# Kernel optimization log

Hardware: AMD Instinct MI355X
Metric: run time of the kernel (lower is better)

The kernel has to match this reference:

```python
import jax, jax.numpy as jnp
import numpy as np
from jax import lax

BS, SL, T = 1024, 512, 64


def setup_inputs() -> dict:
    key = jax.random.key(0)
    k_e, k_tags, k_st, k_et, k_t = jax.random.split(key, 5)
    e = jax.random.normal(k_e, (BS, SL, T), dtype=jnp.float32)
    tags = jax.random.randint(k_tags, (BS, SL), 0, T, dtype=jnp.int32)
    mask = jnp.ones((BS, SL), dtype=bool)
    st = jax.random.uniform(k_st, (T,), minval=-0.1, maxval=0.1, dtype=jnp.float32)
    et = jax.random.uniform(k_et, (T,), minval=-0.1, maxval=0.1, dtype=jnp.float32)
    t = jax.random.uniform(k_t, (T, T), minval=-0.1, maxval=0.1, dtype=jnp.float32)
    return {"e": e, "tags": tags, "mask": mask, "st": st, "et": et, "t": t}


def reference(e, tags, mask, st, et, t):
    # time-major: [sl, bs, T], [sl, bs], [sl, bs]
    e_t = jnp.transpose(e, (1, 0, 2))
    tags_t = tags.T
    mask_t = mask.T
    sl, bs = tags_t.shape
    idx = jnp.arange(bs)

    # gold path score and partition-function init at step 0
    score0 = st[tags_t[0]] + e_t[0, idx, tags_t[0]]          # [bs]
    norm0 = st[None, :] + e_t[0]                              # [bs, T]

    def step(carry, xs):
        score, normalize = carry
        tag_prev, tag_next, e_next, m_next = xs
        mf = m_next.astype(e_next.dtype)
        score = score + (t[tag_prev, tag_next] + e_next[idx, tag_next]) * mf
        # logsumexp over previous tag: [bs, T_prev, T_next] -> [bs, T_next]
        ns = jax.nn.logsumexp(normalize[:, :, None] + t[None, :, :] + e_next[:, None, :], axis=1)
        normalize = jnp.where(m_next[:, None], ns, normalize)
        return (score, normalize), None

    xs = (tags_t[:-1], tags_t[1:], e_t[1:], mask_t[1:])
    (score, normalize), _ = lax.scan(step, (score0, norm0), xs)

    last = mask_t.sum(axis=0) - 1                             # [bs]
    score = score + et[tags_t[last, idx]]
    logZ = jax.nn.logsumexp(normalize + et[None, :], axis=1)  # [bs]
    total = mask.sum().astype(e.dtype)
    return (score - logZ).sum() / total
```

## Files before the change

### kernel.cpp

```cpp
#include <hip/hip_runtime.h>

#define BS 1024
#define SL 512
#define T  64

typedef float v2f __attribute__((ext_vector_type(2)));

__device__ __forceinline__ float wave_reduce_max(float x) {
#pragma unroll
    for (int m = 32; m >= 1; m >>= 1) x = fmaxf(x, __shfl_xor(x, m, 64));
    return x;
}
__device__ __forceinline__ float wave_reduce_sum(float x) {
#pragma unroll
    for (int m = 32; m >= 1; m >>= 1) x += __shfl_xor(x, m, 64);
    return x;
}

#define STEP(S_, EV_)                                                           \
    {                                                                           \
        const int s_ = (S_);                                                    \
        if ((s_ & 63) == 0) tgc = tb[s_ + j];                                   \
        const int tag = __builtin_amdgcn_readlane(tgc, s_ & 63);                \
        const float tv = t[(tag_prev << 6) + tag];                              \
        v2f a0 = {0.f, 0.f}, a1 = {0.f, 0.f}, a2 = {0.f, 0.f}, a3 = {0.f, 0.f}; \
        const int vb_ = __float_as_int(v);                                      \
        _Pragma("unroll")                                                       \
        for (int i = 0; i < T; i += 8) {                                        \
            v2f p0, p1, p2, p3;                                                 \
            p0.x = __int_as_float(__builtin_amdgcn_readlane(vb_, i + 0));       \
            p0.y = __int_as_float(__builtin_amdgcn_readlane(vb_, i + 1));       \
            p1.x = __int_as_float(__builtin_amdgcn_readlane(vb_, i + 2));       \
            p1.y = __int_as_float(__builtin_amdgcn_readlane(vb_, i + 3));       \
            p2.x = __int_as_float(__builtin_amdgcn_readlane(vb_, i + 4));       \
            p2.y = __int_as_float(__builtin_amdgcn_readlane(vb_, i + 5));       \
            p3.x = __int_as_float(__builtin_amdgcn_readlane(vb_, i + 6));       \
            p3.y = __int_as_float(__builtin_amdgcn_readlane(vb_, i + 7));       \
            a0 = __builtin_elementwise_fma(p0, tf2[(i >> 1) + 0], a0);          \
            a1 = __builtin_elementwise_fma(p1, tf2[(i >> 1) + 1], a1);          \
            a2 = __builtin_elementwise_fma(p2, tf2[(i >> 1) + 2], a2);          \
            a3 = __builtin_elementwise_fma(p3, tf2[(i >> 1) + 3], a3);          \
        }                                                                       \
        const float ev_ = (EV_);                                                \
        const float acc_ = ((a0.x + a0.y) + (a1.x + a1.y)) +                    \
                           ((a2.x + a2.y) + (a3.x + a3.y));                     \
        v = acc_ * __expf(ev_);                                                 \
        sc += (j == tag) ? (ev_ + tv) : 0.0f;                                   \
        tag_prev = tag;                                                         \
    }

__global__ __launch_bounds__(64, 1) __attribute__((amdgpu_waves_per_eu(1, 1)))
void crf_fused_kernel(const float* __restrict__ e, const int* __restrict__ tags,
                      const float* __restrict__ st, const float* __restrict__ et,
                      const float* __restrict__ t, float* __restrict__ ws) {
    const int b = blockIdx.x;
    const int j = threadIdx.x;
    const float* eb = e + (size_t)b * (SL * T) + j;
    const int* tb = tags + b * SL;

    v2f tf2[T / 2];
#pragma unroll
    for (int k = 0; k < T / 2; ++k) {
        v2f p;
        p.x = __expf(t[(2 * k) * T + j]);
        p.y = __expf(t[(2 * k + 1) * T + j]);
        tf2[k] = p;
    }

    int tgc = tb[j];
    int tag_prev = __builtin_amdgcn_readlane(tgc, 0);

    const float ev0 = eb[0];
    const float x0 = st[j] + ev0;
    const float m0 = wave_reduce_max(x0);
    float v = __expf(x0 - m0);
    float logscale = m0;
    float sc = (j == 0) ? st[tag_prev] : 0.0f;
    sc += (j == tag_prev) ? ev0 : 0.0f;

    float r0 = eb[1 * T], r1 = eb[2 * T], r2 = eb[3 * T], r3 = eb[4 * T];
    float r4 = eb[5 * T], r5 = eb[6 * T], r6 = eb[7 * T], r7 = eb[8 * T];
    float r8 = eb[9 * T], r9 = eb[10 * T], r10 = eb[11 * T], r11 = eb[12 * T];

    for (int base = 1; base <= SL - 4; base += 4) {
        const int q0 = min(base + 12, SL - 1), q1 = min(base + 13, SL - 1);
        const int q2 = min(base + 14, SL - 1), q3 = min(base + 15, SL - 1);
        const float n0 = eb[(size_t)q0 * T], n1 = eb[(size_t)q1 * T];
        const float n2 = eb[(size_t)q2 * T], n3 = eb[(size_t)q3 * T];

        STEP(base + 0, r0)
        STEP(base + 1, r1)
        STEP(base + 2, r2)
        STEP(base + 3, r3)

        r0 = r4;  r1 = r5;  r2 = r6;  r3 = r7;
        r4 = r8;  r5 = r9;  r6 = r10; r7 = r11;
        r8 = n0;  r9 = n1;  r10 = n2; r11 = n3;

        const int mb = __builtin_amdgcn_readfirstlane(__float_as_int(v));
        const int ex = ((mb >> 23) & 0xff) - 126;
        v *= __int_as_float((127 - ex) << 23);
        logscale += (float)ex * 0.6931471805599453f;
    }
    STEP(509, r0)
    STEP(510, r1)
    STEP(511, r2)

    sc += (j == 0) ? et[tag_prev] : 0.0f;

    const float z = v * __expf(et[j]);
    const float Z = wave_reduce_sum(z);
    const float scs = wave_reduce_sum(sc);
    if (j == 0) ws[b] = scs - (__logf(Z) + logscale);
}

__global__ __launch_bounds__(256)
void final_kernel(const float* __restrict__ ws, float* __restrict__ out) {
    const int tid = threadIdx.x;
    float x = (ws[tid] + ws[tid + 256]) + (ws[tid + 512] + ws[tid + 768]);
    x = wave_reduce_sum(x);
    __shared__ float sm[4];
    if ((tid & 63) == 0) sm[tid >> 6] = x;
    __syncthreads();
    if (tid == 0) out[0] = ((sm[0] + sm[1]) + (sm[2] + sm[3])) / (float)(BS * SL);
}

extern "C" void kernel_launch(void* const* d_in, const int* in_sizes, int n_in,
                              void* d_out, int out_size, void* d_ws, size_t ws_size,
                              hipStream_t stream) {
    const float* e    = (const float*)d_in[0];
    const int*   tags = (const int*)d_in[1];
    const float* st   = (const float*)d_in[3];
    const float* et   = (const float*)d_in[4];
    const float* t    = (const float*)d_in[5];
    float* out = (float*)d_out;
    float* ws  = (float*)d_ws;

    crf_fused_kernel<<<BS, 64, 0, stream>>>(e, tags, st, et, t, ws);
    final_kernel<<<1, 256, 0, stream>>>(ws, out);
}
```

Baseline: 301.7 us.

## Compute CRF forward recurrence matvec with bf16 MFMA instead of readlane FMAs

Replaces the per-step 64x64 scalar matvec, built from readlane broadcasts and packed FMAs, with bf16 16x16x32 MFMA instructions. exp(transitions) is kept in eight bf16 B fragments, and the state vector is re-packed into A fragments each step via ds_bpermute. This is meant to shorten the serial per-step latency of the scan. In exchange it adds an LDS-permute round trip per step and lowers the precision of both the transition matrix and the state to bf16, which can shift the result.

```diff
diff --git a/kernel.cpp b/kernel.cpp
--- a/kernel.cpp
+++ b/kernel.cpp
@@ -1,10 +1,15 @@
 #include <hip/hip_runtime.h>
+#include <hip/hip_bf16.h>
 
 #define BS 1024
 #define SL 512
 #define T  64
 
-typedef float v2f __attribute__((ext_vector_type(2)));
+typedef float f32x4 __attribute__((ext_vector_type(4)));
+typedef short bf16x8 __attribute__((ext_vector_type(8)));
+typedef int   i32x4  __attribute__((ext_vector_type(4)));
+
+union FragU { i32x4 i; bf16x8 v; };
 
 __device__ __forceinline__ float wave_reduce_max(float x) {
 #pragma unroll
@@ -17,36 +22,66 @@
     return x;
 }
 
-#define STEP(S_, EV_)                                                           \
-    {                                                                           \
-        const int s_ = (S_);                                                    \
-        if ((s_ & 63) == 0) tgc = tb[s_ + j];                                   \
-        const int tag = __builtin_amdgcn_readlane(tgc, s_ & 63);                \
-        const float tv = t[(tag_prev << 6) + tag];                              \
-        v2f a0 = {0.f, 0.f}, a1 = {0.f, 0.f}, a2 = {0.f, 0.f}, a3 = {0.f, 0.f}; \
-        const int vb_ = __float_as_int(v);                                      \
-        _Pragma("unroll")                                                       \
-        for (int i = 0; i < T; i += 8) {                                        \
-            v2f p0, p1, p2, p3;                                                 \
-            p0.x = __int_as_float(__builtin_amdgcn_readlane(vb_, i + 0));       \
-            p0.y = __int_as_float(__builtin_amdgcn_readlane(vb_, i + 1));       \
-            p1.x = __int_as_float(__builtin_amdgcn_readlane(vb_, i + 2));       \
-            p1.y = __int_as_float(__builtin_amdgcn_readlane(vb_, i + 3));       \
-            p2.x = __int_as_float(__builtin_amdgcn_readlane(vb_, i + 4));       \
-            p2.y = __int_as_float(__builtin_amdgcn_readlane(vb_, i + 5));       \
-            p3.x = __int_as_float(__builtin_amdgcn_readlane(vb_, i + 6));       \
-            p3.y = __int_as_float(__builtin_amdgcn_readlane(vb_, i + 7));       \
-            a0 = __builtin_elementwise_fma(p0, tf2[(i >> 1) + 0], a0);          \
-            a1 = __builtin_elementwise_fma(p1, tf2[(i >> 1) + 1], a1);          \
-            a2 = __builtin_elementwise_fma(p2, tf2[(i >> 1) + 2], a2);          \
-            a3 = __builtin_elementwise_fma(p3, tf2[(i >> 1) + 3], a3);          \
-        }                                                                       \
-        const float ev_ = (EV_);                                                \
-        const float acc_ = ((a0.x + a0.y) + (a1.x + a1.y)) +                    \
-                           ((a2.x + a2.y) + (a3.x + a3.y));                     \
-        v = acc_ * __expf(ev_);                                                 \
-        sc += (j == tag) ? (ev_ + tv) : 0.0f;                                   \
-        tag_prev = tag;                                                         \
+__device__ __forceinline__ int pk2(float a, float b) {
+    union { __hip_bfloat162 h; int i; } u;
+    u.h = __float22bfloat162_rn(make_float2(a, b));
+    return u.i;
+}
+
+#define MFMA16(A_, B_, C_) __builtin_amdgcn_mfma_f32_16x16x32_bf16((A_), (B_), (C_), 0, 0, 0)
+
+#define STEP(S_, EV_)                                                         \
+    {                                                                         \
+        const int s_ = (S_);                                                  \
+        if ((s_ & 63) == 0) tgc = tb[s_ + j];                                 \
+        const int tag = __builtin_amdgcn_readlane(tgc, s_ & 63);              \
+        const float tv_ = t[(tag_prev << 6) + tag];                           \
+        const float ev_ = (EV_);                                              \
+        const float ge_ = __expf(ev_);                \
+        f32x4 c0 = {0.f, 0.f, 0.f, 0.f}, c1 = {0.f, 0.f, 0.f, 0.f};          \
+        f32x4 c2 = {0.f, 0.f, 0.f, 0.f}, c3 = {0.f, 0.f, 0.f, 0.f};          \
+        c0 = MFMA16(A0, B00, c0); c1 = MFMA16(A0, B01, c1);                   \
+        c2 = MFMA16(A0, B02, c2); c3 = MFMA16(A0, B03, c3);                   \
+        c0 = MFMA16(A1, B10, c0); c1 = MFMA16(A1, B11, c1);                   \
+        c2 = MFMA16(A1, B12, c2); c3 = MFMA16(A1, B13, c3);                   \
+        const float m1_ = (j & 16) ? c1.x : c0.x;                             \
+        const float m2_ = (j & 16) ? c3.x : c2.x;                             \
+        v = ((j & 32) ? m2_ : m1_) * ge_;                 \
+        sc += (j == tag) ? (ev_ + tv_) : 0.0f;                                \
+        tag_prev = tag;                                                      \
+    }
+
+#define BP(OFF_) __int_as_float(__builtin_amdgcn_ds_bpermute(abase + (OFF_), vb_))
+#define REBUILD_A()                                                           \
+    {                                                                         \
+        const int vb_ = __float_as_int(v);                                    \
+        const float p0_ = BP(0),  p1_ = BP(4),  p2_ = BP(8),  p3_ = BP(12);   \
+        const float p4_ = BP(16), p5_ = BP(20), p6_ = BP(24), p7_ = BP(28);   \
+        const float q0_ = BP(128), q1_ = BP(132), q2_ = BP(136), q3_ = BP(140);\
+        const float q4_ = BP(144), q5_ = BP(148), q6_ = BP(152), q7_ = BP(156);\
+        FragU ua_; ua_.i.x = pk2(p0_, p1_); ua_.i.y = pk2(p2_, p3_);          \
+        ua_.i.z = pk2(p4_, p5_); ua_.i.w = pk2(p6_, p7_); A0 = ua_.v;         \
+        FragU ub_; ub_.i.x = pk2(q0_, q1_); ub_.i.y = pk2(q2_, q3_);          \
+        ub_.i.z = pk2(q4_, q5_); ub_.i.w = pk2(q6_, q7_); A1 = ub_.v;         \
+    }
+
+#define RESCALE()                                                             \
+    {                                                                         \
+        const int mb_ = __builtin_amdgcn_readfirstlane(__float_as_int(v));    \
+        const int ex_ = ((mb_ >> 23) & 0xff) - 126;                           \
+        v *= __int_as_float((127 - ex_) << 23);                               \
+        logscale += (float)ex_ * 0.6931471805599453f;                         \
+    }
+
+#define BBUILD(BF_, C_, NT_)                                                  \
+    {                                                                         \
+        const int kb_ = q8 + 32 * (C_), nn_ = nbase + 16 * (NT_);             \
+        FragU u_;                                                             \
+        u_.i.x = pk2(__expf(t[(kb_ + 0) * T + nn_]), __expf(t[(kb_ + 1) * T + nn_])); \
+        u_.i.y = pk2(__expf(t[(kb_ + 2) * T + nn_]), __expf(t[(kb_ + 3) * T + nn_])); \
+        u_.i.z = pk2(__expf(t[(kb_ + 4) * T + nn_]), __expf(t[(kb_ + 5) * T + nn_])); \
+        u_.i.w = pk2(__expf(t[(kb_ + 6) * T + nn_]), __expf(t[(kb_ + 7) * T + nn_])); \
+        BF_ = u_.v;                                                           \
     }
 
 __global__ __launch_bounds__(64, 1) __attribute__((amdgpu_waves_per_eu(1, 1)))
@@ -58,14 +93,13 @@
     const float* eb = e + (size_t)b * (SL * T) + j;
     const int* tb = tags + b * SL;
 
-    v2f tf2[T / 2];
-#pragma unroll
-    for (int k = 0; k < T / 2; ++k) {
-        v2f p;
-        p.x = __expf(t[(2 * k) * T + j]);
-        p.y = __expf(t[(2 * k + 1) * T + j]);
-        tf2[k] = p;
-    }
+    const int q8 = (j >> 4) * 8;
+    const int nbase = j & 15;
+    const int abase = (j & 48) << 1;
+
+    bf16x8 B00, B01, B02, B03, B10, B11, B12, B13;
+    BBUILD(B00, 0, 0) BBUILD(B01, 0, 1) BBUILD(B02, 0, 2) BBUILD(B03, 0, 3)
+    BBUILD(B10, 1, 0) BBUILD(B11, 1, 1) BBUILD(B12, 1, 2) BBUILD(B13, 1, 3)
 
     int tgc = tb[j];
     int tag_prev = __builtin_amdgcn_readlane(tgc, 0);
@@ -78,32 +112,30 @@
     float sc = (j == 0) ? st[tag_prev] : 0.0f;
     sc += (j == tag_prev) ? ev0 : 0.0f;
 
+    bf16x8 A0, A1;
+    REBUILD_A();
+
     float r0 = eb[1 * T], r1 = eb[2 * T], r2 = eb[3 * T], r3 = eb[4 * T];
     float r4 = eb[5 * T], r5 = eb[6 * T], r6 = eb[7 * T], r7 = eb[8 * T];
     float r8 = eb[9 * T], r9 = eb[10 * T], r10 = eb[11 * T], r11 = eb[12 * T];
 
     for (int base = 1; base <= SL - 4; base += 4) {
-        const int q0 = min(base + 12, SL - 1), q1 = min(base + 13, SL - 1);
-        const int q2 = min(base + 14, SL - 1), q3 = min(base + 15, SL - 1);
-        const float n0 = eb[(size_t)q0 * T], n1 = eb[(size_t)q1 * T];
-        const float n2 = eb[(size_t)q2 * T], n3 = eb[(size_t)q3 * T];
+        const int p0 = min(base + 12, SL - 1), p1 = min(base + 13, SL - 1);
+        const int p2 = min(base + 14, SL - 1), p3 = min(base + 15, SL - 1);
+        const float n0 = eb[(size_t)p0 * T], n1 = eb[(size_t)p1 * T];
+        const float n2 = eb[(size_t)p2 * T], n3 = eb[(size_t)p3 * T];
 
-        STEP(base + 0, r0)
-        STEP(base + 1, r1)
-        STEP(base + 2, r2)
-        STEP(base + 3, r3)
+        STEP(base + 0, r0) REBUILD_A();
+        STEP(base + 1, r1) REBUILD_A();
+        STEP(base + 2, r2) REBUILD_A();
+        STEP(base + 3, r3) RESCALE(); REBUILD_A();
 
         r0 = r4;  r1 = r5;  r2 = r6;  r3 = r7;
         r4 = r8;  r5 = r9;  r6 = r10; r7 = r11;
         r8 = n0;  r9 = n1;  r10 = n2; r11 = n3;
-
-        const int mb = __builtin_amdgcn_readfirstlane(__float_as_int(v));
-        const int ex = ((mb >> 23) & 0xff) - 126;
-        v *= __int_as_float((127 - ex) << 23);
-        logscale += (float)ex * 0.6931471805599453f;
     }
-    STEP(509, r0)
-    STEP(510, r1)
+    STEP(509, r0) REBUILD_A();
+    STEP(510, r1) REBUILD_A();
     STEP(511, r2)
 
     sc += (j == 0) ? et[tag_prev] : 0.0f;
```

Result: no change. 296.7 us (-1.7%).
